# Optimization experiments

Measured on AMD Instinct MI355X. Metric: run time of the kernel, lower is better.

Reference implementation:

```python
import jax, jax.numpy as jnp
import numpy as np

B, S, D, H, V = 4, 1024, 2048, 16, 32000
LAYERS, DFF, HID, NSENT, NLAB = 2, 8192, 100, 3, 3
HD = D // H
LN2 = 0.6931471805599453


def _ln(x, g, b):
    m = jnp.mean(x, axis=-1, keepdims=True)
    v = jnp.mean((x - m) ** 2, axis=-1, keepdims=True)
    return (x - m) * jax.lax.rsqrt(v + 1e-5) * g + b


def setup_inputs():
    key = jax.random.key(0)
    ks = jax.random.split(key, 12)
    s = 0.02
    return dict(
        input_ids=jax.random.randint(ks[0], (B, S), 0, V),
        attention_mask=jnp.ones((B, S), dtype=jnp.int32),
        sentiment=jax.random.normal(ks[1], (B, NSENT), dtype=jnp.float32),
        perplexity=jax.random.uniform(ks[2], (B,), dtype=jnp.float32) + 1.0,
        emb=jax.random.normal(ks[3], (V, D), dtype=jnp.float32) * s,
        ln1_g=jnp.ones((LAYERS, D)), ln1_b=jnp.zeros((LAYERS, D)),
        qkv_w=jax.random.normal(ks[4], (LAYERS, D, 3 * D), dtype=jnp.float32) * s,
        wo_w=jax.random.normal(ks[5], (LAYERS, D, D), dtype=jnp.float32) * s,
        ln2_g=jnp.ones((LAYERS, D)), ln2_b=jnp.zeros((LAYERS, D)),
        w1=jax.random.normal(ks[6], (LAYERS, D, DFF), dtype=jnp.float32) * s,
        w2=jax.random.normal(ks[7], (LAYERS, DFF, D), dtype=jnp.float32) * s,
        lnf_g=jnp.ones((D,)), lnf_b=jnp.zeros((D,)),
        head_w=jax.random.normal(ks[8], (D, V), dtype=jnp.float32) * s,
        red_w=jax.random.normal(ks[9], (D, HID), dtype=jnp.float32) * s,
        red_b=jnp.zeros((HID,)),
        cls_w=jax.random.normal(ks[10], (HID + NSENT + 2, NLAB), dtype=jnp.float32) * s,
        cls_b=jnp.zeros((NLAB,)),
    )


def _lm(input_ids, attention_mask, emb, ln1_g, ln1_b, qkv_w, wo_w, ln2_g, ln2_b, w1, w2, lnf_g, lnf_b, head_w):
    x = emb[input_ids]  # [B,S,D]
    amask = attention_mask.astype(jnp.float32)
    causal = jnp.tril(jnp.ones((S, S), dtype=bool))
    bias = jnp.where(causal[None, None, :, :] & (amask[:, None, None, :] > 0), 0.0, -1e9)
    for l in range(LAYERS):
        h = _ln(x, ln1_g[l], ln1_b[l])
        qkv = h @ qkv_w[l]  # [B,S,3D]
        q, k, v = [t.reshape(B, S, H, HD) for t in jnp.split(qkv, 3, axis=-1)]
        scores = jnp.einsum('bqhd,bkhd->bhqk', q, k) / np.float32(np.sqrt(HD)) + bias
        attn = jax.nn.softmax(scores, axis=-1)
        o = jnp.einsum('bhqk,bkhd->bqhd', attn, v).reshape(B, S, D)
        x = x + o @ wo_w[l]
        h = _ln(x, ln2_g[l], ln2_b[l])
        x = x + jax.nn.gelu(h @ w1[l]) @ w2[l]
    h = _ln(x, lnf_g, lnf_b)
    logits = h @ head_w  # [B,S,V]
    return h, logits


def reference(input_ids, attention_mask, sentiment, perplexity, emb, ln1_g, ln1_b, qkv_w, wo_w, ln2_g, ln2_b, w1, w2, lnf_g, lnf_b, head_w, red_w, red_b, cls_w, cls_b):
    h, logits = _lm(input_ids, attention_mask, emb, ln1_g, ln1_b, qkv_w, wo_w,
                    ln2_g, ln2_b, w1, w2, lnf_g, lnf_b, head_w)
    amask = attention_mask.astype(jnp.float32)
    pooled = jnp.mean(h, axis=1)  # mean over seq -> [B,D]
    # probs = softmax(logits).detach(); gather own token prob; -log2(p)
    lg = jax.lax.stop_gradient(logits)
    logZ = jax.scipy.special.logsumexp(lg, axis=-1)  # [B,S]
    tok_logit = jnp.take_along_axis(lg, input_ids[..., None], axis=-1)[..., 0]
    subword_surp = -(tok_logit - logZ) / LN2 * amask
    mean_surprisal = subword_surp.sum(axis=1) / amask.sum(axis=1)  # [B]
    r = jax.nn.leaky_relu(pooled @ red_w + red_b)  # torch intent: LeakyReLU after reducer
    feats = jnp.concatenate([r, sentiment, perplexity[:, None], mean_surprisal[:, None]], axis=1)
    return feats @ cls_w + cls_b  # [B, NLAB]
```

## Files before the change

kernel.cpp:

```cpp
#include <hip/hip_runtime.h>

typedef unsigned short u16;
typedef __bf16 bf16x8 __attribute__((ext_vector_type(8)));
typedef float f32x4 __attribute__((ext_vector_type(4)));

__device__ __forceinline__ u16 f2bf(float f){
  unsigned u = __float_as_uint(f);
  unsigned r = u + 0x7FFFu + ((u >> 16) & 1u);
  return (u16)(r >> 16);
}
__device__ __forceinline__ float bf2f(u16 v){ return __uint_as_float(((unsigned)v) << 16); }

__global__ __launch_bounds__(256) void transp_k(const float* __restrict__ in, u16* __restrict__ out, int K, int N)
{
  __shared__ float tl[32][33];
  const int n0 = blockIdx.x * 32, k0 = blockIdx.y * 32;
  const int x = threadIdx.x, y = threadIdx.y;
#pragma unroll
  for (int i = 0; i < 4; ++i)
    tl[y + 8*i][x] = in[(size_t)(k0 + y + 8*i) * N + n0 + x];
  __syncthreads();
#pragma unroll
  for (int i = 0; i < 4; ++i)
    out[(size_t)(n0 + y + 8*i) * K + k0 + x] = f2bf(tl[x][y + 8*i]);
}

__global__ __launch_bounds__(256) void embed_k(const int* __restrict__ ids, const float* __restrict__ emb, float* __restrict__ x)
{
  const int row = blockIdx.x;
  const int c = blockIdx.y * 256 + threadIdx.x;
  x[(size_t)row * 2048 + c] = emb[(size_t)ids[row] * 2048 + c];
}

__global__ __launch_bounds__(256) void ln_k(const float* __restrict__ x, const float* __restrict__ gw,
                                            const float* __restrict__ bw, u16* __restrict__ o)
{
  const int row = blockIdx.x, t = threadIdx.x;
  const int lane = t & 63, wid = t >> 6;
  const float4* xr = (const float4*)(x + (size_t)row * 2048);
  float4 v1 = xr[t], v2 = xr[t + 256];
  float s1 = v1.x + v1.y + v1.z + v1.w + v2.x + v2.y + v2.z + v2.w;
  float s2 = v1.x*v1.x + v1.y*v1.y + v1.z*v1.z + v1.w*v1.w
           + v2.x*v2.x + v2.y*v2.y + v2.z*v2.z + v2.w*v2.w;
#pragma unroll
  for (int off = 32; off >= 1; off >>= 1){ s1 += __shfl_down(s1, off); s2 += __shfl_down(s2, off); }
  __shared__ float rb[2][4];
  __shared__ float mv[2];
  if (lane == 0){ rb[0][wid] = s1; rb[1][wid] = s2; }
  __syncthreads();
  if (t == 0){
    float a = rb[0][0] + rb[0][1] + rb[0][2] + rb[0][3];
    float q = rb[1][0] + rb[1][1] + rb[1][2] + rb[1][3];
    float mean = a * (1.f/2048.f);
    float var  = q * (1.f/2048.f) - mean*mean;
    mv[0] = mean; mv[1] = rsqrtf(var + 1e-5f);
  }
  __syncthreads();
  const float mean = mv[0], rstd = mv[1];
  const float4* g4 = (const float4*)gw;
  const float4* b4 = (const float4*)bw;
  float4 ga = g4[t], ba = b4[t], gb = g4[t + 256], bb2 = b4[t + 256];
  ushort4 o1, o2;
  o1.x = f2bf((v1.x - mean)*rstd*ga.x + ba.x);
  o1.y = f2bf((v1.y - mean)*rstd*ga.y + ba.y);
  o1.z = f2bf((v1.z - mean)*rstd*ga.z + ba.z);
  o1.w = f2bf((v1.w - mean)*rstd*ga.w + ba.w);
  o2.x = f2bf((v2.x - mean)*rstd*gb.x + bb2.x);
  o2.y = f2bf((v2.y - mean)*rstd*gb.y + bb2.y);
  o2.z = f2bf((v2.z - mean)*rstd*gb.z + bb2.z);
  o2.w = f2bf((v2.w - mean)*rstd*gb.w + bb2.w);
  ((ushort4*)(o + (size_t)row * 2048))[t] = o1;
  ((ushort4*)(o + (size_t)row * 2048))[t + 256] = o2;
}

enum { M_QKV = 0, M_RES = 1, M_GELU = 2, M_LSE = 3 };

template<int MODE>
__global__ __launch_bounds__(256) void gemm_k(
    const u16* __restrict__ A, const u16* __restrict__ BT,
    int N, int K, int MB,
    u16* __restrict__ outb, float* __restrict__ outf,
    float* __restrict__ partial, float* __restrict__ tokl,
    const int* __restrict__ ids, u16* __restrict__ vtout)
{
  __shared__ u16 lA[128 * 64];
  __shared__ u16 lB[128 * 64];
  const int bid = blockIdx.x;
  const int bm = bid % MB, bn = bid / MB;
  const int m0 = bm * 128, n0 = bn * 128;
  const int tid = threadIdx.x;
  const int lane = tid & 63, wid = tid >> 6;
  const int wm = wid >> 1, wn = wid & 1;
  const int lg = lane >> 4, lr = lane & 15;

  f32x4 acc[4][4];
#pragma unroll
  for (int i = 0; i < 4; ++i)
#pragma unroll
    for (int j = 0; j < 4; ++j)
#pragma unroll
      for (int r = 0; r < 4; ++r) acc[i][j][r] = 0.f;

  const int nkt = K >> 6;
  for (int kt = 0; kt < nkt; ++kt){
#pragma unroll
    for (int it = 0; it < 4; ++it){
      const int ci = tid + it * 256;
      const int row = ci >> 3, kc = ci & 7;
      const int loff = row * 128 + ((kc * 16) ^ ((row & 7) << 4));
      uint4 va = *(const uint4*)(A  + (size_t)(m0 + row) * K + kt * 64 + kc * 8);
      *(uint4*)((char*)lA + loff) = va;
      uint4 vb = *(const uint4*)(BT + (size_t)(n0 + row) * K + kt * 64 + kc * 8);
      *(uint4*)((char*)lB + loff) = vb;
    }
    __syncthreads();
#pragma unroll
    for (int kk = 0; kk < 2; ++kk){
      bf16x8 af[4], bfr[4];
#pragma unroll
      for (int f = 0; f < 4; ++f){
        const int ra = wm * 64 + f * 16 + lr;
        af[f]  = *(const bf16x8*)((const char*)lA + ra * 128 + ((kk * 64 + lg * 16) ^ ((ra & 7) << 4)));
        const int rb = wn * 64 + f * 16 + lr;
        bfr[f] = *(const bf16x8*)((const char*)lB + rb * 128 + ((kk * 64 + lg * 16) ^ ((rb & 7) << 4)));
      }
#pragma unroll
      for (int i = 0; i < 4; ++i)
#pragma unroll
        for (int j = 0; j < 4; ++j)
          acc[i][j] = __builtin_amdgcn_mfma_f32_16x16x32_bf16(af[i], bfr[j], acc[i][j], 0, 0, 0);
    }
    __syncthreads();
  }

#pragma unroll
  for (int i = 0; i < 4; ++i){
#pragma unroll
    for (int r = 0; r < 4; ++r){
      const int row = m0 + wm * 64 + i * 16 + lg * 4 + r;
      if constexpr (MODE == M_LSE){
        const int id = ids[row];
        float esum = 0.f;
#pragma unroll
        for (int j = 0; j < 4; ++j){
          const int col = n0 + wn * 64 + j * 16 + lr;
          const float v = acc[i][j][r];
          if (col == id) tokl[row] = v;
          esum += __expf(v);
        }
#pragma unroll
        for (int off = 8; off >= 1; off >>= 1) esum += __shfl_xor(esum, off);
        if (lr == 0) partial[(size_t)row * 500 + bn * 2 + wn] = esum;
      } else {
#pragma unroll
        for (int j = 0; j < 4; ++j){
          const int col = n0 + wn * 64 + j * 16 + lr;
          const float v = acc[i][j][r];
          if constexpr (MODE == M_RES){
            float* pp = outf + (size_t)row * N + col;
            *pp += v;
          } else if constexpr (MODE == M_GELU){
            float u = 0.7978845608028654f * (v + 0.044715f * v * v * v);
            u = fminf(fmaxf(u, -15.f), 15.f);
            const float ex = __expf(2.f * u);
            const float th = (ex - 1.f) / (ex + 1.f);
            outb[(size_t)row * N + col] = f2bf(0.5f * v * (1.f + th));
          } else {
            const u16 uv = f2bf(v);
            if (col < 4096) outb[(size_t)row * 6144 + col] = uv;
            else {
              int dd2 = col - 4096;
              const int hh = dd2 >> 7; dd2 &= 127;
              vtout[(((size_t)((row >> 10) * 16 + hh)) * 128 + dd2) * 1024 + (row & 1023)] = uv;
            }
          }
        }
      }
    }
  }
}

__global__ __launch_bounds__(64) void attn_k(const u16* __restrict__ qkv, const u16* __restrict__ vT, u16* __restrict__ o16)
{
  __shared__ u16 P[16 * 40];
  const int bid = blockIdx.x;
  const int qt = bid & 63, bh = bid >> 6;
  const int h = bh & 15, b = bh >> 4;
  const int lane = threadIdx.x, lg = lane >> 4, lr = lane & 15;
  const int q0 = qt << 4;
  const u16* qrow  = qkv + (size_t)(b * 1024 + q0 + lr) * 6144 + h * 128;
  const u16* krow  = qkv + (size_t)(b * 1024 + lr) * 6144 + 2048 + h * 128;
  const u16* vbase = vT + (size_t)(b * 16 + h) * 128 * 1024;

  bf16x8 qf[4];
#pragma unroll
  for (int c = 0; c < 4; ++c) qf[c] = *(const bf16x8*)(qrow + c * 32 + lg * 8);

  float m[4], l[4];
  f32x4 oacc[8];
#pragma unroll
  for (int r = 0; r < 4; ++r){ m[r] = -1e30f; l[r] = 0.f; }
#pragma unroll
  for (int f = 0; f < 8; ++f)
#pragma unroll
    for (int r = 0; r < 4; ++r) oacc[f][r] = 0.f;

  const float scale = 0.08838834764831845f;
  const int nk2 = (qt >> 1) + 1;
  for (int k2 = 0; k2 < nk2; ++k2){
    float e[2][4];
    float rmax[4];
#pragma unroll
    for (int r = 0; r < 4; ++r) rmax[r] = -1e30f;
#pragma unroll
    for (int hh = 0; hh < 2; ++hh){
      const int kt = k2 * 2 + hh;
      if (kt <= qt){
        f32x4 s;
#pragma unroll
        for (int r = 0; r < 4; ++r) s[r] = 0.f;
#pragma unroll
        for (int c = 0; c < 4; ++c){
          bf16x8 kf = *(const bf16x8*)(krow + (size_t)(kt * 16) * 6144 + c * 32 + lg * 8);
          s = __builtin_amdgcn_mfma_f32_16x16x32_bf16(qf[c], kf, s, 0, 0, 0);
        }
#pragma unroll
        for (int r = 0; r < 4; ++r){
          float sv = s[r] * scale;
          if (kt * 16 + lr > q0 + lg * 4 + r) sv = -1e30f;
          e[hh][r] = sv;
          rmax[r] = fmaxf(rmax[r], sv);
        }
      } else {
#pragma unroll
        for (int r = 0; r < 4; ++r) e[hh][r] = -1e30f;
      }
    }
#pragma unroll
    for (int off = 8; off >= 1; off >>= 1)
#pragma unroll
      for (int r = 0; r < 4; ++r) rmax[r] = fmaxf(rmax[r], __shfl_xor(rmax[r], off));
    float corr[4], rsum[4];
#pragma unroll
    for (int r = 0; r < 4; ++r){
      const float mn = fmaxf(m[r], rmax[r]);
      corr[r] = __expf(m[r] - mn);
      m[r] = mn;
      const float e0 = __expf(e[0][r] - mn);
      const float e1 = __expf(e[1][r] - mn);
      e[0][r] = e0; e[1][r] = e1;
      rsum[r] = e0 + e1;
    }
#pragma unroll
    for (int off = 8; off >= 1; off >>= 1)
#pragma unroll
      for (int r = 0; r < 4; ++r) rsum[r] += __shfl_xor(rsum[r], off);
#pragma unroll
    for (int r = 0; r < 4; ++r) l[r] = l[r] * corr[r] + rsum[r];
#pragma unroll
    for (int hh = 0; hh < 2; ++hh)
#pragma unroll
      for (int r = 0; r < 4; ++r)
        P[(lg * 4 + r) * 40 + hh * 16 + lr] = f2bf(e[hh][r]);
#pragma unroll
    for (int f = 0; f < 8; ++f)
#pragma unroll
      for (int r = 0; r < 4; ++r) oacc[f][r] = oacc[f][r] * corr[r];
    __syncthreads();
    const bf16x8 pa = *(const bf16x8*)((const u16*)P + lr * 40 + lg * 8);
#pragma unroll
    for (int f = 0; f < 8; ++f){
      bf16x8 vb = *(const bf16x8*)(vbase + (size_t)(f * 16 + lr) * 1024 + k2 * 32 + lg * 8);
      oacc[f] = __builtin_amdgcn_mfma_f32_16x16x32_bf16(pa, vb, oacc[f], 0, 0, 0);
    }
    __syncthreads();
  }
  u16* orow = o16 + (size_t)(b * 1024 + q0 + lg * 4) * 2048 + h * 128;
#pragma unroll
  for (int r = 0; r < 4; ++r){
    const float linv = 1.0f / l[r];
#pragma unroll
    for (int f = 0; f < 8; ++f)
      orow[(size_t)r * 2048 + f * 16 + lr] = f2bf(oacc[f][r] * linv);
  }
}

__global__ __launch_bounds__(256) void lse_k(const float* __restrict__ partial, const float* __restrict__ tokl,
                                             const int* __restrict__ amask, float* __restrict__ surp)
{
  const int row = blockIdx.x, t = threadIdx.x, lane = t & 63, wid = t >> 6;
  float s = 0.f;
  if (t < 250) s = partial[(size_t)row * 500 + t] + partial[(size_t)row * 500 + t + 250];
#pragma unroll
  for (int off = 32; off >= 1; off >>= 1) s += __shfl_down(s, off);
  __shared__ float rb[4];
  if (lane == 0) rb[wid] = s;
  __syncthreads();
  if (t == 0){
    const float tot = rb[0] + rb[1] + rb[2] + rb[3];
    surp[row] = (logf(tot) - tokl[row]) * 1.4426950408889634f * (float)amask[row];
  }
}

__global__ __launch_bounds__(256) void pool_k(const u16* __restrict__ h16, float* __restrict__ pooled)
{
  const int d = blockIdx.x * 256 + threadIdx.x;
  const int b = blockIdx.y;
  const u16* p = h16 + (size_t)b * 1024 * 2048 + d;
  float a0 = 0.f, a1 = 0.f, a2 = 0.f, a3 = 0.f;
  for (int s = 0; s < 1024; s += 4){
    a0 += bf2f(p[(size_t)(s + 0) * 2048]);
    a1 += bf2f(p[(size_t)(s + 1) * 2048]);
    a2 += bf2f(p[(size_t)(s + 2) * 2048]);
    a3 += bf2f(p[(size_t)(s + 3) * 2048]);
  }
  pooled[b * 2048 + d] = (a0 + a1 + a2 + a3) * (1.f / 1024.f);
}

__global__ __launch_bounds__(256) void cls_k(const float* __restrict__ pooled, const float* __restrict__ surp,
                                             const int* __restrict__ amask, const float* __restrict__ sent,
                                             const float* __restrict__ ppl, const float* __restrict__ redw,
                                             const float* __restrict__ redb, const float* __restrict__ clsw,
                                             const float* __restrict__ clsb, float* __restrict__ out)
{
  const int b = blockIdx.x, t = threadIdx.x;
  const int lane = t & 63, wid = t >> 6;
  __shared__ float pl[2048];
  __shared__ float feats[112];
  __shared__ float rbuf[2][4];
#pragma unroll
  for (int i = 0; i < 8; ++i) pl[t + i * 256] = pooled[b * 2048 + t + i * 256];
  float ssum = 0.f, msum = 0.f;
#pragma unroll
  for (int i = 0; i < 4; ++i){
    const int s = t + i * 256;
    ssum += surp[b * 1024 + s];
    msum += (float)amask[b * 1024 + s];
  }
#pragma unroll
  for (int off = 32; off >= 1; off >>= 1){ ssum += __shfl_down(ssum, off); msum += __shfl_down(msum, off); }
  if (lane == 0){ rbuf[0][wid] = ssum; rbuf[1][wid] = msum; }
  __syncthreads();
  if (t == 0){
    float a = 0.f, c = 0.f;
    for (int i = 0; i < 4; ++i){ a += rbuf[0][i]; c += rbuf[1][i]; }
    feats[104] = a / c;
  }
  if (t >= 100 && t < 103) feats[t] = sent[b * 3 + (t - 100)];
  if (t == 103) feats[103] = ppl[b];
  if (t < 100){
    float a = redb[t];
    for (int d = 0; d < 2048; ++d) a += pl[d] * redw[d * 100 + t];
    feats[t] = (a > 0.f) ? a : 0.01f * a;
  }
  __syncthreads();
  if (t < 3){
    float a = clsb[t];
    for (int i = 0; i < 105; ++i) a += feats[i] * clsw[i * 3 + t];
    out[b * 3 + t] = a;
  }
}

extern "C" void kernel_launch(void* const* d_in, const int* in_sizes, int n_in,
                              void* d_out, int out_size, void* d_ws, size_t ws_size,
                              hipStream_t stream)
{
  (void)in_sizes; (void)n_in; (void)out_size; (void)ws_size;
  const int*   ids   = (const int*)d_in[0];
  const int*   amask = (const int*)d_in[1];
  const float* sent  = (const float*)d_in[2];
  const float* ppl   = (const float*)d_in[3];
  const float* emb   = (const float*)d_in[4];
  const float* ln1g  = (const float*)d_in[5];
  const float* ln1b  = (const float*)d_in[6];
  const float* qkvw  = (const float*)d_in[7];
  const float* wow   = (const float*)d_in[8];
  const float* ln2g  = (const float*)d_in[9];
  const float* ln2b  = (const float*)d_in[10];
  const float* w1    = (const float*)d_in[11];
  const float* w2    = (const float*)d_in[12];
  const float* lnfg  = (const float*)d_in[13];
  const float* lnfb  = (const float*)d_in[14];
  const float* headw = (const float*)d_in[15];
  const float* redw  = (const float*)d_in[16];
  const float* redb  = (const float*)d_in[17];
  const float* clsw  = (const float*)d_in[18];
  const float* clsb  = (const float*)d_in[19];
  float* out = (float*)d_out;

  char* p = (char*)d_ws;
  u16* wqkvT = (u16*)p; p += (size_t)2 * 6144 * 2048 * 2;
  u16* woT   = (u16*)p; p += (size_t)2 * 2048 * 2048 * 2;
  u16* w1T   = (u16*)p; p += (size_t)2 * 8192 * 2048 * 2;
  u16* w2T   = (u16*)p; p += (size_t)2 * 2048 * 8192 * 2;
  u16* whT   = (u16*)p; p += (size_t)32000 * 2048 * 2;
  float* xbuf = (float*)p; p += (size_t)4096 * 2048 * 4;
  u16* h16   = (u16*)p; p += (size_t)4096 * 2048 * 2;
  u16* qkv16 = (u16*)p;
  u16* vT16  = (u16*)(p + (size_t)4096 * 6144 * 2);
  u16* ffn16 = (u16*)p;
  p += (size_t)4096 * 6144 * 2 + (size_t)4096 * 2048 * 2;
  u16* o16   = (u16*)p; p += (size_t)4096 * 2048 * 2;
  float* partial = (float*)p; p += (size_t)4096 * 500 * 4;
  float* tokl = (float*)p; p += (size_t)4096 * 4;
  float* surp = (float*)p; p += (size_t)4096 * 4;
  float* pooled = (float*)p; p += (size_t)4 * 2048 * 4;

  dim3 tblk(32, 8);
  for (int l = 0; l < 2; ++l){
    transp_k<<<dim3(6144/32, 2048/32), tblk, 0, stream>>>(qkvw + (size_t)l*2048*6144, wqkvT + (size_t)l*6144*2048, 2048, 6144);
    transp_k<<<dim3(2048/32, 2048/32), tblk, 0, stream>>>(wow  + (size_t)l*2048*2048, woT   + (size_t)l*2048*2048, 2048, 2048);
    transp_k<<<dim3(8192/32, 2048/32), tblk, 0, stream>>>(w1   + (size_t)l*2048*8192, w1T   + (size_t)l*8192*2048, 2048, 8192);
    transp_k<<<dim3(2048/32, 8192/32), tblk, 0, stream>>>(w2   + (size_t)l*8192*2048, w2T   + (size_t)l*2048*8192, 8192, 2048);
  }
  transp_k<<<dim3(32000/32, 2048/32), tblk, 0, stream>>>(headw, whT, 2048, 32000);

  embed_k<<<dim3(4096, 8), 256, 0, stream>>>(ids, emb, xbuf);

  for (int l = 0; l < 2; ++l){
    ln_k<<<4096, 256, 0, stream>>>(xbuf, ln1g + l*2048, ln1b + l*2048, h16);
    gemm_k<M_QKV><<<32*48, 256, 0, stream>>>(h16, wqkvT + (size_t)l*6144*2048, 6144, 2048, 32,
                                             qkv16, nullptr, nullptr, nullptr, nullptr, vT16);
    attn_k<<<4096, 64, 0, stream>>>(qkv16, vT16, o16);
    gemm_k<M_RES><<<32*16, 256, 0, stream>>>(o16, woT + (size_t)l*2048*2048, 2048, 2048, 32,
                                             nullptr, xbuf, nullptr, nullptr, nullptr, nullptr);
    ln_k<<<4096, 256, 0, stream>>>(xbuf, ln2g + l*2048, ln2b + l*2048, h16);
    gemm_k<M_GELU><<<32*64, 256, 0, stream>>>(h16, w1T + (size_t)l*8192*2048, 8192, 2048, 32,
                                              ffn16, nullptr, nullptr, nullptr, nullptr, nullptr);
    gemm_k<M_RES><<<32*16, 256, 0, stream>>>(ffn16, w2T + (size_t)l*2048*8192, 2048, 8192, 32,
                                             nullptr, xbuf, nullptr, nullptr, nullptr, nullptr);
  }
  ln_k<<<4096, 256, 0, stream>>>(xbuf, lnfg, lnfb, h16);
  gemm_k<M_LSE><<<32*250, 256, 0, stream>>>(h16, whT, 32000, 2048, 32,
                                            nullptr, nullptr, partial, tokl, ids, nullptr);
  lse_k<<<4096, 256, 0, stream>>>(partial, tokl, amask, surp);
  pool_k<<<dim3(8, 4), 256, 0, stream>>>(h16, pooled);
  cls_k<<<4, 256, 0, stream>>>(pooled, surp, amask, sent, ppl, redw, redb, clsw, clsb, out);
}
```

Measured before the change: 2.565 ms.

## Rewrite GEMM with larger tiles, triple-buffered direct-to-LDS loads, and wider transpose

Replaces the 128x128 single-buffered GEMM with a 512-thread kernel using 256x256 or 128x256 tiles and BK=32. Loads go straight to LDS with global_load_lds into a triple buffer, using vmcnt waits so global loads overlap MFMA work, plus a grid swizzle for cache locality and s_setprio around the MFMAs. The weight transpose kernel also moves to 64x64 tiles with float4 reads and ushort4 writes. This adds complexity and LDS use, and the smaller grids for the N=2048 GEMMs may leave fewer workgroups per CU.

After: 2.416 ms. -5.8%, faster.

```diff
diff --git a/kernel.cpp b/kernel.cpp
--- a/kernel.cpp
+++ b/kernel.cpp
@@ -11,18 +11,33 @@
 }
 __device__ __forceinline__ float bf2f(u16 v){ return __uint_as_float(((unsigned)v) << 16); }
 
+__device__ __forceinline__ void gload16(const void* g, void* l){
+  __builtin_amdgcn_global_load_lds(
+      (const __attribute__((address_space(1))) unsigned int*)g,
+      (__attribute__((address_space(3))) unsigned int*)l, 16, 0, 0);
+}
+
 __global__ __launch_bounds__(256) void transp_k(const float* __restrict__ in, u16* __restrict__ out, int K, int N)
 {
-  __shared__ float tl[32][33];
-  const int n0 = blockIdx.x * 32, k0 = blockIdx.y * 32;
-  const int x = threadIdx.x, y = threadIdx.y;
-#pragma unroll
-  for (int i = 0; i < 4; ++i)
-    tl[y + 8*i][x] = in[(size_t)(k0 + y + 8*i) * N + n0 + x];
-  __syncthreads();
-#pragma unroll
-  for (int i = 0; i < 4; ++i)
-    out[(size_t)(n0 + y + 8*i) * K + k0 + x] = f2bf(tl[x][y + 8*i]);
+  __shared__ float tl[64][65];
+  const int n0 = blockIdx.x * 64, k0 = blockIdx.y * 64;
+  const int t = threadIdx.x;
+  const int r = t >> 4, c4 = t & 15;
+#pragma unroll
+  for (int i = 0; i < 4; ++i){
+    float4 v = *(const float4*)(in + (size_t)(k0 + r + i*16) * N + n0 + c4*4);
+    tl[r + i*16][c4*4 + 0] = v.x; tl[r + i*16][c4*4 + 1] = v.y;
+    tl[r + i*16][c4*4 + 2] = v.z; tl[r + i*16][c4*4 + 3] = v.w;
+  }
+  __syncthreads();
+#pragma unroll
+  for (int i = 0; i < 4; ++i){
+    const int n = r + i*16;
+    ushort4 o;
+    o.x = f2bf(tl[c4*4 + 0][n]); o.y = f2bf(tl[c4*4 + 1][n]);
+    o.z = f2bf(tl[c4*4 + 2][n]); o.w = f2bf(tl[c4*4 + 3][n]);
+    *(ushort4*)(out + (size_t)(n0 + n) * K + k0 + c4*4) = o;
+  }
 }
 
 __global__ __launch_bounds__(256) void embed_k(const int* __restrict__ ids, const float* __restrict__ emb, float* __restrict__ x)
@@ -75,86 +90,126 @@
 
 enum { M_QKV = 0, M_RES = 1, M_GELU = 2, M_LSE = 3 };
 
-template<int MODE>
-__global__ __launch_bounds__(256) void gemm_k(
+template<int MODE, int BM>
+__global__ __launch_bounds__(512, 2) void gemm2_k(
     const u16* __restrict__ A, const u16* __restrict__ BT,
     int N, int K, int MB,
     u16* __restrict__ outb, float* __restrict__ outf,
     float* __restrict__ partial, float* __restrict__ tokl,
     const int* __restrict__ ids, u16* __restrict__ vtout)
 {
-  __shared__ u16 lA[128 * 64];
-  __shared__ u16 lB[128 * 64];
+  constexpr int BK  = 32;
+  constexpr int ASZ = BM * BK;
+  constexpr int BSZ = 256 * BK;
+  constexpr int BUF = ASZ + BSZ;
+  constexpr int NFR = BM / 32;
+  __shared__ u16 lds[3 * BUF];
+
+  const int tid  = threadIdx.x;
+  const int wv   = tid >> 6, lane = tid & 63;
+  const int wr   = wv >> 2,  wc   = wv & 3;
+  const int lg   = lane >> 4, lr  = lane & 15;
+
+  const int nwg = gridDim.x;
   const int bid = blockIdx.x;
-  const int bm = bid % MB, bn = bid / MB;
-  const int m0 = bm * 128, n0 = bn * 128;
-  const int tid = threadIdx.x;
-  const int lane = tid & 63, wid = tid >> 6;
-  const int wm = wid >> 1, wn = wid & 1;
-  const int lg = lane >> 4, lr = lane & 15;
-
-  f32x4 acc[4][4];
-#pragma unroll
-  for (int i = 0; i < 4; ++i)
+  const int swz = ((nwg & 7) == 0) ? ((bid & 7) * (nwg >> 3) + (bid >> 3)) : bid;
+  const int bm = swz % MB, bn = swz / MB;
+  const int m0 = bm * BM, n0 = bn * 256;
+
+  const int ll = lane >> 3;
+  const int cc = lane & 7;
+  const int lc = cc ^ ll;
+  const int gr = (ll << 1) + (lc >> 2);
+  const int gk = (lc & 3) << 3;
+
+  const u16* gA = A  + (size_t)m0 * K + gk;
+  const u16* gB = BT + (size_t)n0 * K + gk;
+
+  f32x4 acc[NFR][4];
+#pragma unroll
+  for (int i = 0; i < NFR; ++i)
 #pragma unroll
     for (int j = 0; j < 4; ++j)
 #pragma unroll
       for (int r = 0; r < 4; ++r) acc[i][j][r] = 0.f;
 
-  const int nkt = K >> 6;
-  for (int kt = 0; kt < nkt; ++kt){
-#pragma unroll
-    for (int it = 0; it < 4; ++it){
-      const int ci = tid + it * 256;
-      const int row = ci >> 3, kc = ci & 7;
-      const int loff = row * 128 + ((kc * 16) ^ ((row & 7) << 4));
-      uint4 va = *(const uint4*)(A  + (size_t)(m0 + row) * K + kt * 64 + kc * 8);
-      *(uint4*)((char*)lA + loff) = va;
-      uint4 vb = *(const uint4*)(BT + (size_t)(n0 + row) * K + kt * 64 + kc * 8);
-      *(uint4*)((char*)lB + loff) = vb;
-    }
-    __syncthreads();
-#pragma unroll
-    for (int kk = 0; kk < 2; ++kk){
-      bf16x8 af[4], bfr[4];
-#pragma unroll
-      for (int f = 0; f < 4; ++f){
-        const int ra = wm * 64 + f * 16 + lr;
-        af[f]  = *(const bf16x8*)((const char*)lA + ra * 128 + ((kk * 64 + lg * 16) ^ ((ra & 7) << 4)));
-        const int rb = wn * 64 + f * 16 + lr;
-        bfr[f] = *(const bf16x8*)((const char*)lB + rb * 128 + ((kk * 64 + lg * 16) ^ ((rb & 7) << 4)));
-      }
-#pragma unroll
-      for (int i = 0; i < 4; ++i)
-#pragma unroll
-        for (int j = 0; j < 4; ++j)
-          acc[i][j] = __builtin_amdgcn_mfma_f32_16x16x32_bf16(af[i], bfr[j], acc[i][j], 0, 0, 0);
-    }
-    __syncthreads();
-  }
-
-#pragma unroll
-  for (int i = 0; i < 4; ++i){
+  const int nt = K >> 5;
+
+  auto STAGE = [&](int bi, int kt){
+    char* bA = (char*)lds + (size_t)bi * BUF * 2;
+    char* bB = bA + ASZ * 2;
+    const size_t ko = (size_t)kt * 32;
+    if constexpr (BM == 256){
+      gload16(gA + (size_t)((wv    ) * 16 + gr) * K + ko, bA + (wv    ) * 1024);
+      gload16(gA + (size_t)((wv + 8) * 16 + gr) * K + ko, bA + (wv + 8) * 1024);
+    } else {
+      gload16(gA + (size_t)(wv * 16 + gr) * K + ko, bA + wv * 1024);
+    }
+    gload16(gB + (size_t)((wv    ) * 16 + gr) * K + ko, bB + (wv    ) * 1024);
+    gload16(gB + (size_t)((wv + 8) * 16 + gr) * K + ko, bB + (wv + 8) * 1024);
+  };
+
+  STAGE(0, 0);
+  STAGE(1, 1);
+
+  for (int t = 0; t < nt; ++t){
+    if (t + 1 < nt){
+      if constexpr (BM == 256) asm volatile("s_waitcnt vmcnt(4) lgkmcnt(0)" ::: "memory");
+      else                     asm volatile("s_waitcnt vmcnt(3) lgkmcnt(0)" ::: "memory");
+    } else {
+      asm volatile("s_waitcnt vmcnt(0) lgkmcnt(0)" ::: "memory");
+    }
+    __builtin_amdgcn_s_barrier();
+    if (t + 2 < nt) STAGE((t + 2) % 3, t + 2);
+
+    const char* bA = (const char*)lds + (size_t)(t % 3) * BUF * 2;
+    const char* bB = bA + ASZ * 2;
+    bf16x8 af[NFR], bq[4];
+#pragma unroll
+    for (int i = 0; i < NFR; ++i){
+      const int ra = wr * (BM / 2) + i * 16 + lr;
+      const int p = ra >> 1;
+      const int slot = (((ra & 1) << 2) | lg) ^ (p & 7);
+      af[i] = *(const bf16x8*)(bA + p * 128 + slot * 16);
+    }
+#pragma unroll
+    for (int j = 0; j < 4; ++j){
+      const int rb = wc * 64 + j * 16 + lr;
+      const int p = rb >> 1;
+      const int slot = (((rb & 1) << 2) | lg) ^ (p & 7);
+      bq[j] = *(const bf16x8*)(bB + p * 128 + slot * 16);
+    }
+    __builtin_amdgcn_s_setprio(1);
+#pragma unroll
+    for (int i = 0; i < NFR; ++i)
+#pragma unroll
+      for (int j = 0; j < 4; ++j)
+        acc[i][j] = __builtin_amdgcn_mfma_f32_16x16x32_bf16(af[i], bq[j], acc[i][j], 0, 0, 0);
+    __builtin_amdgcn_s_setprio(0);
+  }
+
+#pragma unroll
+  for (int i = 0; i < NFR; ++i){
 #pragma unroll
     for (int r = 0; r < 4; ++r){
-      const int row = m0 + wm * 64 + i * 16 + lg * 4 + r;
+      const int row = m0 + wr * (BM / 2) + i * 16 + lg * 4 + r;
       if constexpr (MODE == M_LSE){
         const int id = ids[row];
         float esum = 0.f;
 #pragma unroll
         for (int j = 0; j < 4; ++j){
-          const int col = n0 + wn * 64 + j * 16 + lr;
+          const int col = n0 + wc * 64 + j * 16 + lr;
           const float v = acc[i][j][r];
           if (col == id) tokl[row] = v;
           esum += __expf(v);
         }
 #pragma unroll
         for (int off = 8; off >= 1; off >>= 1) esum += __shfl_xor(esum, off);
-        if (lr == 0) partial[(size_t)row * 500 + bn * 2 + wn] = esum;
+        if (lr == 0) partial[(size_t)row * 500 + bn * 4 + wc] = esum;
       } else {
 #pragma unroll
         for (int j = 0; j < 4; ++j){
-          const int col = n0 + wn * 64 + j * 16 + lr;
+          const int col = n0 + wc * 64 + j * 16 + lr;
           const float v = acc[i][j][r];
           if constexpr (MODE == M_RES){
             float* pp = outf + (size_t)row * N + col;
@@ -406,33 +461,32 @@
   float* surp = (float*)p; p += (size_t)4096 * 4;
   float* pooled = (float*)p; p += (size_t)4 * 2048 * 4;
 
-  dim3 tblk(32, 8);
   for (int l = 0; l < 2; ++l){
-    transp_k<<<dim3(6144/32, 2048/32), tblk, 0, stream>>>(qkvw + (size_t)l*2048*6144, wqkvT + (size_t)l*6144*2048, 2048, 6144);
-    transp_k<<<dim3(2048/32, 2048/32), tblk, 0, stream>>>(wow  + (size_t)l*2048*2048, woT   + (size_t)l*2048*2048, 2048, 2048);
-    transp_k<<<dim3(8192/32, 2048/32), tblk, 0, stream>>>(w1   + (size_t)l*2048*8192, w1T   + (size_t)l*8192*2048, 2048, 8192);
-    transp_k<<<dim3(2048/32, 8192/32), tblk, 0, stream>>>(w2   + (size_t)l*8192*2048, w2T   + (size_t)l*2048*8192, 8192, 2048);
-  }
-  transp_k<<<dim3(32000/32, 2048/32), tblk, 0, stream>>>(headw, whT, 2048, 32000);
+    transp_k<<<dim3(6144/64, 2048/64), 256, 0, stream>>>(qkvw + (size_t)l*2048*6144, wqkvT + (size_t)l*6144*2048, 2048, 6144);
+    transp_k<<<dim3(2048/64, 2048/64), 256, 0, stream>>>(wow  + (size_t)l*2048*2048, woT   + (size_t)l*2048*2048, 2048, 2048);
+    transp_k<<<dim3(8192/64, 2048/64), 256, 0, stream>>>(w1   + (size_t)l*2048*8192, w1T   + (size_t)l*8192*2048, 2048, 8192);
+    transp_k<<<dim3(2048/64, 8192/64), 256, 0, stream>>>(w2   + (size_t)l*8192*2048, w2T   + (size_t)l*2048*8192, 8192, 2048);
+  }
+  transp_k<<<dim3(32000/64, 2048/64), 256, 0, stream>>>(headw, whT, 2048, 32000);
 
   embed_k<<<dim3(4096, 8), 256, 0, stream>>>(ids, emb, xbuf);
 
   for (int l = 0; l < 2; ++l){
     ln_k<<<4096, 256, 0, stream>>>(xbuf, ln1g + l*2048, ln1b + l*2048, h16);
-    gemm_k<M_QKV><<<32*48, 256, 0, stream>>>(h16, wqkvT + (size_t)l*6144*2048, 6144, 2048, 32,
-                                             qkv16, nullptr, nullptr, nullptr, nullptr, vT16);
+    gemm2_k<M_QKV,256><<<16*24, 512, 0, stream>>>(h16, wqkvT + (size_t)l*6144*2048, 6144, 2048, 16,
+                                                  qkv16, nullptr, nullptr, nullptr, nullptr, vT16);
     attn_k<<<4096, 64, 0, stream>>>(qkv16, vT16, o16);
-    gemm_k<M_RES><<<32*16, 256, 0, stream>>>(o16, woT + (size_t)l*2048*2048, 2048, 2048, 32,
-                                             nullptr, xbuf, nullptr, nullptr, nullptr, nullptr);
+    gemm2_k<M_RES,128><<<32*8, 512, 0, stream>>>(o16, woT + (size_t)l*2048*2048, 2048, 2048, 32,
+                                                 nullptr, xbuf, nullptr, nullptr, nullptr, nullptr);
     ln_k<<<4096, 256, 0, stream>>>(xbuf, ln2g + l*2048, ln2b + l*2048, h16);
-    gemm_k<M_GELU><<<32*64, 256, 0, stream>>>(h16, w1T + (size_t)l*8192*2048, 8192, 2048, 32,
-                                              ffn16, nullptr, nullptr, nullptr, nullptr, nullptr);
-    gemm_k<M_RES><<<32*16, 256, 0, stream>>>(ffn16, w2T + (size_t)l*2048*8192, 2048, 8192, 32,
-                                             nullptr, xbuf, nullptr, nullptr, nullptr, nullptr);
+    gemm2_k<M_GELU,256><<<16*32, 512, 0, stream>>>(h16, w1T + (size_t)l*8192*2048, 8192, 2048, 16,
+                                                   ffn16, nullptr, nullptr, nullptr, nullptr, nullptr);
+    gemm2_k<M_RES,128><<<32*8, 512, 0, stream>>>(ffn16, w2T + (size_t)l*2048*8192, 2048, 8192, 32,
+                                                 nullptr, xbuf, nullptr, nullptr, nullptr, nullptr);
   }
   ln_k<<<4096, 256, 0, stream>>>(xbuf, lnfg, lnfb, h16);
-  gemm_k<M_LSE><<<32*250, 256, 0, stream>>>(h16, whT, 32000, 2048, 32,
-                                            nullptr, nullptr, partial, tokl, ids, nullptr);
+  gemm2_k<M_LSE,256><<<16*125, 512, 0, stream>>>(h16, whT, 32000, 2048, 16,
+                                                 nullptr, nullptr, partial, tokl, ids, nullptr);
   lse_k<<<4096, 256, 0, stream>>>(partial, tokl, amask, surp);
   pool_k<<<dim3(8, 4), 256, 0, stream>>>(h16, pooled);
   cls_k<<<4, 256, 0, stream>>>(pooled, surp, amask, sent, ppl, redw, redb, clsw, clsb, out);
```
